# Performance work log

Measured on AMD Instinct MI355X. Metric: run time of the kernel, lower is better.

Reference implementation:

```python
import jax, jax.numpy as jnp
import numpy as np

B, S, D = 16, 1024, 128
V = 100000
N = 4096


def _l2norm(x, eps=1e-12):
    # matches torch F.normalize(dim=-1): x / max(||x||, eps)
    n = jnp.sqrt(jnp.sum(x * x, axis=-1, keepdims=True))
    return x / jnp.maximum(n, eps)


def setup_inputs() -> dict:
    key = jax.random.key(0)
    k1, k2, k3, k4, k5 = jax.random.split(key, 5)
    query_embeddings = jax.random.normal(k1, (B, S, D), dtype=jnp.float32)
    key_embeddings = jax.random.normal(k2, (V, D), dtype=jnp.float32)
    loc_b = jax.random.randint(k3, (N,), 0, B)
    loc_s = jax.random.randint(k4, (N,), 0, S)
    label_locations = jnp.stack([loc_b, loc_s], axis=1).astype(jnp.int64)
    labels = jax.random.randint(k5, (N,), 0, V).astype(jnp.int64)
    return {
        "query_embeddings": query_embeddings,
        "key_embeddings": key_embeddings,
        "label_locations": label_locations,
        "labels": labels,
    }


def reference(query_embeddings, key_embeddings, label_locations, labels):
    # gather query vectors at label positions -> [N, D]
    q = query_embeddings[label_locations[:, 0], label_locations[:, 1]]
    q = _l2norm(q)
    k = _l2norm(key_embeddings)
    logits = jnp.einsum("nd,vd->nv", q, k)  # [N, V]
    logZ = jax.nn.logsumexp(logits, axis=-1)  # [N]
    true_logit = jnp.take_along_axis(logits, labels[:, None], axis=-1)[:, 0]
    loss = jnp.mean(logZ - true_logit)  # CrossEntropyLoss mean reduction
    return loss
```

## Files before the change

kernel.cpp:

```cpp
#include <hip/hip_runtime.h>
#include <hip/hip_bf16.h>
#include <hip/hip_fp8.h>

#define S_ 1024
#define D_ 128
#define V_ 100000
#define VSTRIPS_ 3136
#define NPHASE_ 64
#define N_ 4096
#define PADROWS_ 352.0f

typedef __attribute__((ext_vector_type(4))) float f32x4;
typedef __attribute__((ext_vector_type(4))) int   i32x4;
typedef __attribute__((ext_vector_type(8))) int   i32x8;

#define LOG2E_ 1.4426950408889634f
#define LN2_   0.6931471805599453f

__device__ __forceinline__ float exp2_fast(float x) {
#if __has_builtin(__builtin_amdgcn_exp2f)
    return __builtin_amdgcn_exp2f(x);
#else
    return exp2f(x);
#endif
}

__device__ __forceinline__ unsigned char to_fp8(float x) {
    __hip_fp8_e4m3 t(x);
    return (unsigned char)t.__x;
}
__device__ __forceinline__ float from_fp8(unsigned char b) {
    __hip_fp8_e4m3 t; t.__x = (__hip_fp8_storage_t)b;
    return (float)t;
}

__global__ void prep_kernel(const float* __restrict__ K, const float* __restrict__ Q,
                            const int* __restrict__ loc,
                            char* __restrict__ Kn, char* __restrict__ Qn,
                            float* __restrict__ Ssum) {
    __shared__ char sm[4096];
    const int bid = blockIdx.x;
    const int tid = threadIdx.x;
    const int lane = tid & 63;
    const int wvv = tid >> 6;
    if (bid < VSTRIPS_) {
        char* dst = Kn + (size_t)bid * 4096;
        if (bid >= 3125) {
            *(f32x4*)(dst + tid * 16) = (f32x4){0.f, 0.f, 0.f, 0.f};
            return;
        }
        #pragma unroll
        for (int i = 0; i < 8; ++i) {
            int r = wvv * 8 + i;
            float2 v = ((const float2*)(K + ((size_t)bid * 32 + r) * D_))[lane];
            float ss = v.x * v.x + v.y * v.y;
            #pragma unroll
            for (int off = 32; off; off >>= 1) ss += __shfl_xor(ss, off);
            float rn = rsqrtf(ss);
            unsigned short pk = (unsigned short)to_fp8(v.x * rn)
                              | ((unsigned short)to_fp8(v.y * rn) << 8);
            int addr = ((r >> 4) << 11) + (((lane >> 4) * 16 + (r & 15)) << 5)
                     + ((lane & 15) << 1);
            *(unsigned short*)(sm + addr) = pk;
        }
        __syncthreads();
        *(f32x4*)(dst + tid * 16) = *(const f32x4*)(sm + tid * 16);
    } else {
        int w = (bid - VSTRIPS_) * 4 + wvv;
        if (lane == 0) Ssum[w] = 0.f;
        int b = loc[2 * w], s = loc[2 * w + 1];
        float2 v = ((const float2*)(Q + ((size_t)b * S_ + (size_t)s) * D_))[lane];
        float ss = v.x * v.x + v.y * v.y;
        #pragma unroll
        for (int off = 32; off; off >>= 1) ss += __shfl_xor(ss, off);
        float rn = rsqrtf(ss) * LOG2E_;
        unsigned short pk = (unsigned short)to_fp8(v.x * rn)
                          | ((unsigned short)to_fp8(v.y * rn) << 8);
        *(unsigned short*)(Qn + (size_t)w * 128 + 2 * lane) = pk;
    }
}

__global__ __launch_bounds__(256, 2) void ce_main(
    const char* __restrict__ Qn,
    const char* __restrict__ Kn,
    float* __restrict__ Ssum)
{
    const int tid  = threadIdx.x;
    const int lane = tid & 63;
    const int wv   = tid >> 6;
    const int r0   = lane & 15;
    const int hi   = lane >> 4;

    const int fid   = blockIdx.y * 16 + blockIdx.x;
    const int xcd   = fid & 7;
    const int idx   = fid >> 3;
    const int phase = xcd * 8 + (idx >> 4);
    const int qb    = idx & 15;

    i32x8 afr[4];
    {
        const char* qsrc = Qn + ((size_t)qb * 256 + wv * 64 + r0) * 128 + (hi << 5);
        #pragma unroll
        for (int m = 0; m < 4; ++m)
            afr[m] = *(const i32x8*)(qsrc + m * 2048);
    }

    const char* kvbase = Kn + (size_t)phase * 4096 + (lane << 5);

#define LOADSET(B0, B1, j) do {                                              \
        const char* p = kvbase + (size_t)(j) * (4096 * NPHASE_);             \
        B0 = *(const i32x8*)(p);                                             \
        B1 = *(const i32x8*)(p + 2048);                                      \
    } while (0)

#define COMPUTE(B0, B1, ACC) do {                                            \
        _Pragma("unroll")                                                    \
        for (int m = 0; m < 4; ++m) {                                        \
            ACC[m][0] = __builtin_amdgcn_mfma_scale_f32_16x16x128_f8f6f4(    \
                afr[m], B0, fz, 0, 0, 0, 127, 0, 127);                       \
            ACC[m][1] = __builtin_amdgcn_mfma_scale_f32_16x16x128_f8f6f4(    \
                afr[m], B1, fz, 0, 0, 0, 127, 0, 127);                       \
        }                                                                    \
    } while (0)

#define EXP2S(ACC) do {                                                      \
        _Pragma("unroll")                                                    \
        for (int m = 0; m < 4; ++m)                                          \
            _Pragma("unroll")                                                \
            for (int q = 0; q < 4; ++q)                                      \
                psum[m][q] += exp2_fast(ACC[m][0][q]) + exp2_fast(ACC[m][1][q]); \
    } while (0)

    float psum[4][4];
    #pragma unroll
    for (int m = 0; m < 4; ++m)
        #pragma unroll
        for (int q = 0; q < 4; ++q) psum[m][q] = 0.f;

    const f32x4 fz = {0.f, 0.f, 0.f, 0.f};
    f32x4 accE[4][2], accO[4][2];
    #pragma unroll
    for (int m = 0; m < 4; ++m)
        #pragma unroll
        for (int nn = 0; nn < 2; ++nn)
            accO[m][nn] = (f32x4){-16384.f, -16384.f, -16384.f, -16384.f};

    i32x8 RA0, RA1, RB0, RB1;
    LOADSET(RA0, RA1, 0);
    #pragma unroll 1
    for (int j = 0; j < 48; j += 2) {
        LOADSET(RB0, RB1, j + 1);
        EXP2S(accO);
        COMPUTE(RA0, RA1, accE);
        LOADSET(RA0, RA1, j + 2);
        EXP2S(accE);
        COMPUTE(RB0, RB1, accO);
    }
    EXP2S(accO);
    COMPUTE(RA0, RA1, accE);
    EXP2S(accE);

#undef LOADSET
#undef COMPUTE
#undef EXP2S

    #pragma unroll
    for (int m = 0; m < 4; ++m) {
        #pragma unroll
        for (int q = 0; q < 4; ++q) {
            float v = psum[m][q];
            v += __shfl_xor(v, 1);
            v += __shfl_xor(v, 2);
            v += __shfl_xor(v, 4);
            v += __shfl_xor(v, 8);
            if (r0 == 0) {
                int row = qb * 256 + wv * 64 + m * 16 + hi * 4 + q;
                atomicAdd(&Ssum[row], v);
            }
        }
    }
}

__global__ void term_kernel(const char* __restrict__ Qn,
                            const char* __restrict__ Kn,
                            const int* __restrict__ labels,
                            const float* __restrict__ Ssum,
                            float* __restrict__ T) {
    int w = (blockIdx.x * blockDim.x + threadIdx.x) >> 6;
    int lane = threadIdx.x & 63;
    if (w >= N_) return;
    int lab = labels[w];
    const unsigned char* qp = (const unsigned char*)(Qn + (size_t)w * 128 + 2 * lane);
    const unsigned char* kp = (const unsigned char*)(Kn
                      + ((size_t)(lab >> 5)) * 4096 + (((lab >> 4) & 1) << 11)
                      + (((lane >> 4) * 16 + (lab & 15)) << 5) + ((lane & 15) << 1));
    float d = from_fp8(qp[0]) * from_fp8(kp[0])
            + from_fp8(qp[1]) * from_fp8(kp[1]);
    #pragma unroll
    for (int off = 32; off; off >>= 1) d += __shfl_xor(d, off);
    if (lane == 0) T[w] = logf(Ssum[w] - PADROWS_) - d * LN2_;
}

__global__ void reduce_kernel(const float* __restrict__ T, float* __restrict__ out) {
    __shared__ float sm[4];
    float s = 0.f;
    for (int i = threadIdx.x; i < N_; i += 256) s += T[i];
    #pragma unroll
    for (int off = 32; off; off >>= 1) s += __shfl_xor(s, off);
    if ((threadIdx.x & 63) == 0) sm[threadIdx.x >> 6] = s;
    __syncthreads();
    if (threadIdx.x == 0) out[0] = (sm[0] + sm[1] + sm[2] + sm[3]) * (1.0f / (float)N_);
}

extern "C" void kernel_launch(void* const* d_in, const int* in_sizes, int n_in,
                              void* d_out, int out_size, void* d_ws, size_t ws_size,
                              hipStream_t stream) {
    (void)in_sizes; (void)n_in; (void)out_size; (void)ws_size;
    const float* Q   = (const float*)d_in[0];
    const float* K   = (const float*)d_in[1];
    const int* loc   = (const int*)d_in[2];
    const int* labels= (const int*)d_in[3];
    float* out = (float*)d_out;

    char* ws = (char*)d_ws;
    char* Kn    = ws;
    char* Qn    = ws + 12845056;
    float* Ssum = (float*)(ws + 12845056 + 524288);
    float* T    = Ssum + N_;

    prep_kernel<<<VSTRIPS_ + N_ / 4, 256, 0, stream>>>(K, Q, loc, Kn, Qn, Ssum);
    ce_main<<<dim3(16, NPHASE_), 256, 0, stream>>>(Qn, Kn, Ssum);
    term_kernel<<<N_ / 4, 256, 0, stream>>>(Qn, Kn, labels, Ssum, T);
    reduce_kernel<<<1, 256, 0, stream>>>(T, out);
}
```

Baseline: 78.53 us.

## Warp-specialize ce_main into MFMA producer and exp2 consumer waves via LDS

The main kernel now launches 512 threads per block. Four waves compute the fp8 MFMA logits tiles and write the accumulators into a double-buffered 64KB LDS area. The other four waves read those tiles, apply exp2, accumulate row sums and do the final atomic adds. The aim is to overlap matrix-core work with transcendental work on separate waves. In exchange it adds LDS traffic, a block-wide barrier every step, and drops to one block per CU.

```diff
diff --git a/kernel.cpp b/kernel.cpp
--- a/kernel.cpp
+++ b/kernel.cpp
@@ -80,14 +80,17 @@
     }
 }
 
-__global__ __launch_bounds__(256, 2) void ce_main(
+__global__ __launch_bounds__(512, 1) void ce_main(
     const char* __restrict__ Qn,
     const char* __restrict__ Kn,
     float* __restrict__ Ssum)
 {
+    __shared__ char lbuf[65536];
+
     const int tid  = threadIdx.x;
     const int lane = tid & 63;
     const int wv   = tid >> 6;
+    const int p    = wv & 3;
     const int r0   = lane & 15;
     const int hi   = lane >> 4;
 
@@ -97,85 +100,105 @@
     const int phase = xcd * 8 + (idx >> 4);
     const int qb    = idx & 15;
 
-    i32x8 afr[4];
-    {
-        const char* qsrc = Qn + ((size_t)qb * 256 + wv * 64 + r0) * 128 + (hi << 5);
-        #pragma unroll
-        for (int m = 0; m < 4; ++m)
-            afr[m] = *(const i32x8*)(qsrc + m * 2048);
-    }
-
-    const char* kvbase = Kn + (size_t)phase * 4096 + (lane << 5);
+    const int loff = (p << 13) + (lane << 4);
+
+    if (wv < 4) {
+        i32x8 afr[4];
+        {
+            const char* qsrc = Qn + ((size_t)qb * 256 + p * 64 + r0) * 128 + (hi << 5);
+            #pragma unroll
+            for (int m = 0; m < 4; ++m)
+                afr[m] = *(const i32x8*)(qsrc + m * 2048);
+        }
+        const char* kvbase = Kn + (size_t)phase * 4096 + (lane << 5);
+        const f32x4 fz = {0.f, 0.f, 0.f, 0.f};
+        f32x4 acc[4][2];
+        i32x8 RA0, RA1, RB0, RB1;
 
 #define LOADSET(B0, B1, j) do {                                              \
-        const char* p = kvbase + (size_t)(j) * (4096 * NPHASE_);             \
-        B0 = *(const i32x8*)(p);                                             \
-        B1 = *(const i32x8*)(p + 2048);                                      \
-    } while (0)
-
-#define COMPUTE(B0, B1, ACC) do {                                            \
+        const char* pp = kvbase + (size_t)(j) * (4096 * NPHASE_);            \
+        B0 = *(const i32x8*)(pp);                                            \
+        B1 = *(const i32x8*)(pp + 2048);                                     \
+    } while (0)
+
+#define COMPUTE(B0, B1) do {                                                 \
         _Pragma("unroll")                                                    \
         for (int m = 0; m < 4; ++m) {                                        \
-            ACC[m][0] = __builtin_amdgcn_mfma_scale_f32_16x16x128_f8f6f4(    \
+            acc[m][0] = __builtin_amdgcn_mfma_scale_f32_16x16x128_f8f6f4(    \
                 afr[m], B0, fz, 0, 0, 0, 127, 0, 127);                       \
-            ACC[m][1] = __builtin_amdgcn_mfma_scale_f32_16x16x128_f8f6f4(    \
+            acc[m][1] = __builtin_amdgcn_mfma_scale_f32_16x16x128_f8f6f4(    \
                 afr[m], B1, fz, 0, 0, 0, 127, 0, 127);                       \
         }                                                                    \
     } while (0)
 
-#define EXP2S(ACC) do {                                                      \
+#define WRITEACC(OFF) do {                                                   \
         _Pragma("unroll")                                                    \
         for (int m = 0; m < 4; ++m)                                          \
             _Pragma("unroll")                                                \
-            for (int q = 0; q < 4; ++q)                                      \
-                psum[m][q] += exp2_fast(ACC[m][0][q]) + exp2_fast(ACC[m][1][q]); \
-    } while (0)
-
-    float psum[4][4];
-    #pragma unroll
-    for (int m = 0; m < 4; ++m)
-        #pragma unroll
-        for (int q = 0; q < 4; ++q) psum[m][q] = 0.f;
-
-    const f32x4 fz = {0.f, 0.f, 0.f, 0.f};
-    f32x4 accE[4][2], accO[4][2];
-    #pragma unroll
-    for (int m = 0; m < 4; ++m)
-        #pragma unroll
-        for (int nn = 0; nn < 2; ++nn)
-            accO[m][nn] = (f32x4){-16384.f, -16384.f, -16384.f, -16384.f};
-
-    i32x8 RA0, RA1, RB0, RB1;
-    LOADSET(RA0, RA1, 0);
-    #pragma unroll 1
-    for (int j = 0; j < 48; j += 2) {
-        LOADSET(RB0, RB1, j + 1);
-        EXP2S(accO);
-        COMPUTE(RA0, RA1, accE);
-        LOADSET(RA0, RA1, j + 2);
-        EXP2S(accE);
-        COMPUTE(RB0, RB1, accO);
-    }
-    EXP2S(accO);
-    COMPUTE(RA0, RA1, accE);
-    EXP2S(accE);
-
+            for (int nn = 0; nn < 2; ++nn)                                   \
+                *(f32x4*)(lbuf + (OFF) + loff + ((m * 2 + nn) << 10)) = acc[m][nn]; \
+    } while (0)
+
+        LOADSET(RA0, RA1, 0);
+        #pragma unroll 1
+        for (int j = 0; j < 48; j += 2) {
+            LOADSET(RB0, RB1, j + 1);
+            COMPUTE(RA0, RA1);
+            WRITEACC(0);
+            __syncthreads();
+            LOADSET(RA0, RA1, j + 2);
+            COMPUTE(RB0, RB1);
+            WRITEACC(32768);
+            __syncthreads();
+        }
+        COMPUTE(RA0, RA1);
+        WRITEACC(0);
+        __syncthreads();
 #undef LOADSET
 #undef COMPUTE
-#undef EXP2S
-
-    #pragma unroll
-    for (int m = 0; m < 4; ++m) {
-        #pragma unroll
-        for (int q = 0; q < 4; ++q) {
-            float v = psum[m][q];
-            v += __shfl_xor(v, 1);
-            v += __shfl_xor(v, 2);
-            v += __shfl_xor(v, 4);
-            v += __shfl_xor(v, 8);
-            if (r0 == 0) {
-                int row = qb * 256 + wv * 64 + m * 16 + hi * 4 + q;
-                atomicAdd(&Ssum[row], v);
+#undef WRITEACC
+    } else {
+        float psum[4][4];
+        #pragma unroll
+        for (int m = 0; m < 4; ++m)
+            #pragma unroll
+            for (int q = 0; q < 4; ++q) psum[m][q] = 0.f;
+
+#define READEXP(OFF) do {                                                    \
+        _Pragma("unroll")                                                    \
+        for (int m = 0; m < 4; ++m) {                                        \
+            f32x4 v0 = *(const f32x4*)(lbuf + (OFF) + loff + ((m * 2) << 10));       \
+            f32x4 v1 = *(const f32x4*)(lbuf + (OFF) + loff + ((m * 2 + 1) << 10));   \
+            _Pragma("unroll")                                                \
+            for (int q = 0; q < 4; ++q)                                      \
+                psum[m][q] += exp2_fast(v0[q]) + exp2_fast(v1[q]);           \
+        }                                                                    \
+    } while (0)
+
+        #pragma unroll 1
+        for (int j = 0; j < 48; j += 2) {
+            __syncthreads();
+            READEXP(0);
+            __syncthreads();
+            READEXP(32768);
+        }
+        __syncthreads();
+        READEXP(0);
+#undef READEXP
+
+        #pragma unroll
+        for (int m = 0; m < 4; ++m) {
+            #pragma unroll
+            for (int q = 0; q < 4; ++q) {
+                float v = psum[m][q];
+                v += __shfl_xor(v, 1);
+                v += __shfl_xor(v, 2);
+                v += __shfl_xor(v, 4);
+                v += __shfl_xor(v, 8);
+                if (r0 == 0) {
+                    int row = qb * 256 + p * 64 + m * 16 + hi * 4 + q;
+                    atomicAdd(&Ssum[row], v);
+                }
             }
         }
     }
@@ -229,7 +252,7 @@
     float* T    = Ssum + N_;
 
     prep_kernel<<<VSTRIPS_ + N_ / 4, 256, 0, stream>>>(K, Q, loc, Kn, Qn, Ssum);
-    ce_main<<<dim3(16, NPHASE_), 256, 0, stream>>>(Qn, Kn, Ssum);
+    ce_main<<<dim3(16, NPHASE_), 512, 0, stream>>>(Qn, Kn, Ssum);
     term_kernel<<<N_ / 4, 256, 0, stream>>>(Qn, Kn, labels, Ssum, T);
     reduce_kernel<<<1, 256, 0, stream>>>(T, out);
 }
```

New measurement: 93.82 us. +19.5%, slower.
